# Kernel tuning notes

Measured on AMD Instinct MI355X. Metric: run time of the kernel, lower is better.

## Reference

```python
import jax, jax.numpy as jnp
import numpy as np

EPS = 1e-12  # matches torch F.normalize default eps


def setup_inputs() -> dict:
    key = jax.random.key(0)
    k_x, k_w1, k_b1, k_w2, k_b2 = jax.random.split(key, 5)
    b, n, r, d = 8, 64, 256, 512
    return {
        "x": jax.random.normal(k_x, (b, n, r, d), dtype=jnp.float32),
        "W1": jax.random.normal(k_w1, (d, d), dtype=jnp.float32) * (1.0 / np.sqrt(d)),
        "b1": jax.random.normal(k_b1, (d,), dtype=jnp.float32) * 0.01,
        "W2": jax.random.normal(k_w2, (1, d), dtype=jnp.float32) * (1.0 / np.sqrt(d)),
        "b2": jax.random.normal(k_b2, (1,), dtype=jnp.float32) * 0.01,
    }


def reference(x, W1, b1, W2, b2):
    # F.normalize(x, dim=-1): x / max(||x||_2, eps)
    norm = jnp.sqrt(jnp.sum(x * x, axis=-1, keepdims=True))
    xn = x / jnp.maximum(norm, EPS)                      # [b,n,r,d]
    h = jnp.tanh(jnp.einsum('bnrd,ed->bnre', xn, W1) + b1)  # linear1 + tanh
    scores = (jnp.einsum('bnrd,od->bnro', h, W2) + b2)[..., 0]  # [b,n,r]
    alphas = jax.nn.softmax(scores, axis=2)              # softmax over regions r
    fbar = jnp.einsum('bnr,bnrd->bnd', alphas, xn)       # weighted pooling
    return (fbar, alphas)
```

## Files before the change

### kernel.cpp

```cpp
#include <hip/hip_runtime.h>
#include <hip/hip_bf16.h>

typedef short short8 __attribute__((ext_vector_type(8)));
typedef float floatx4 __attribute__((ext_vector_type(4)));

#define NGROUP 512
#define RREG 256
#define D 512
#define ROWS 131072
#define FBAR_ELEMS (NGROUP * D)

__device__ __forceinline__ unsigned short f2bf(float f) {
    unsigned int u = __float_as_uint(f);
    unsigned int r = (u + 0x7fffu + ((u >> 16) & 1u)) >> 16;
    return (unsigned short)r;
}
__device__ __forceinline__ float fast_tanh(float x) {
    float cx = fminf(fmaxf(x, -9.5f), 9.5f);
    float e  = __builtin_amdgcn_exp2f(cx * 2.8853900817779268f);
    return (e - 1.f) * __builtin_amdgcn_rcpf(e + 1.f);
}

__global__ __launch_bounds__(256) void conv_w1(const float* __restrict__ W1,
                                               unsigned short* __restrict__ W1c) {
    int tid = blockIdx.x * 256 + threadIdx.x;
    int P = tid * 8;
    int kc = P >> 15;
    int L = P & 32767;
    int col = L >> 6;
    int q = L & 63;
    int kl = (q ^ (((col >> 1) & 3) << 4)) >> 1;
    const float* src = W1 + col * 512 + kc * 32 + kl;
    float4 v = *reinterpret_cast<const float4*>(src);
    ushort4 o;
    o.x = f2bf(v.x); o.y = f2bf(v.y); o.z = f2bf(v.z); o.w = f2bf(v.w);
    *reinterpret_cast<ushort4*>((char*)W1c + P) = o;
}

__global__ __launch_bounds__(1024, 8) void score_gemm(
    const float* __restrict__ x, const unsigned short* __restrict__ W1c,
    const float* __restrict__ b1, const float* __restrict__ W2v,
    float* __restrict__ inv_norm, float* __restrict__ scores) {

    __shared__ unsigned short A_lds[2][64 * 32];
    __shared__ unsigned short B_lds[2][512 * 32];
    __shared__ float inv_s[64];

    const int t = threadIdx.x;
    const int lane = t & 63;
    const int w = t >> 6;
    const int cl = lane & 15;
    const int hi = lane >> 4;
    const size_t row0 = (size_t)blockIdx.x * 64;

    auto stageB = [&](int buf, int kc) {
        const char* gb = (const char*)W1c + kc * 32768 + w * 2048 + lane * 16;
        char* lb = (char*)B_lds[buf] + w * 2048;
        #pragma unroll
        for (int i = 0; i < 2; ++i) {
            __builtin_amdgcn_global_load_lds(
                (const __attribute__((address_space(1))) void*)(gb + i * 1024),
                (__attribute__((address_space(3))) void*)(lb + i * 1024),
                16, 0, 0);
        }
    };

    const int arow = t >> 4;
    const int kq = t & 15;
    const int abyte = arow * 64 + ((kq * 4) ^ (((arow >> 1) & 3) << 4));
    const float* xp = x + (row0 + arow) * (size_t)D + kq * 2;

    float ssacc = 0.f;
    auto packA = [&](int buf, float2 v) {
        ssacc += v.x * v.x + v.y * v.y;
        unsigned int pk = (unsigned int)f2bf(v.x) | ((unsigned int)f2bf(v.y) << 16);
        *reinterpret_cast<unsigned int*>((char*)A_lds[buf] + abyte) = pk;
    };

    stageB(0, 0);
    packA(0, *reinterpret_cast<const float2*>(xp));
    __syncthreads();

    floatx4 acc[4][2];
    #pragma unroll
    for (int tt = 0; tt < 4; ++tt) {
        acc[tt][0] = floatx4{0, 0, 0, 0};
        acc[tt][1] = floatx4{0, 0, 0, 0};
    }

    const int fofs = (hi * 16) ^ (((cl >> 1) & 3) << 4);

    #pragma unroll 2
    for (int s = 0; s < 16; ++s) {
        const int cur = s & 1, nx = cur ^ 1;

        float2 xv;
        if (s < 15) {
            xv = *reinterpret_cast<const float2*>(xp + (s + 1) * 32);
            stageB(nx, s + 1);
        }

        short8 bfr0 = *reinterpret_cast<const short8*>(
            (char*)B_lds[cur] + (w * 32 + cl) * 64 + fofs);
        short8 bfr1 = *reinterpret_cast<const short8*>(
            (char*)B_lds[cur] + (w * 32 + 16 + cl) * 64 + fofs);
        #pragma unroll
        for (int tt = 0; tt < 4; ++tt) {
            short8 afr = *reinterpret_cast<const short8*>(
                (char*)A_lds[cur] + (tt * 16 + cl) * 64 + fofs);
            acc[tt][0] = __builtin_amdgcn_mfma_f32_16x16x32_bf16(afr, bfr0, acc[tt][0], 0, 0, 0);
            acc[tt][1] = __builtin_amdgcn_mfma_f32_16x16x32_bf16(afr, bfr1, acc[tt][1], 0, 0, 0);
        }

        if (s < 15) {
            packA(nx, xv);
            __syncthreads();
        }
    }

    ssacc += __shfl_xor(ssacc, 1, 16);
    ssacc += __shfl_xor(ssacc, 2, 16);
    ssacc += __shfl_xor(ssacc, 4, 16);
    ssacc += __shfl_xor(ssacc, 8, 16);
    if (kq == 0) {
        float inv = 1.0f / fmaxf(sqrtf(ssacc), 1e-12f);
        inv_s[arow] = inv;
        inv_norm[row0 + arow] = inv;
    }
    __syncthreads();

    float* scorebuf = (float*)A_lds;

    #pragma unroll
    for (int tt = 0; tt < 4; ++tt) {
        floatx4 iv = *reinterpret_cast<const floatx4*>(&inv_s[tt * 16 + hi * 4]);
        float sp[4] = {0.f, 0.f, 0.f, 0.f};
        #pragma unroll
        for (int f = 0; f < 2; ++f) {
            int col = w * 32 + f * 16 + cl;
            float wv = W2v[col];
            float bb = b1[col];
            #pragma unroll
            for (int i = 0; i < 4; ++i)
                sp[i] += wv * fast_tanh(acc[tt][f][i] * iv[i] + bb);
        }
        #pragma unroll
        for (int i = 0; i < 4; ++i) {
            float v = sp[i];
            v += __shfl_xor(v, 1, 64);
            v += __shfl_xor(v, 2, 64);
            v += __shfl_xor(v, 4, 64);
            v += __shfl_xor(v, 8, 64);
            if (cl == 0) scorebuf[w * 64 + tt * 16 + hi * 4 + i] = v;
        }
    }
    __syncthreads();

    if (t < 64) {
        float s = 0.f;
        #pragma unroll
        for (int q = 0; q < 16; ++q) s += scorebuf[q * 64 + t];
        scores[row0 + t] = s;
    }
}

__global__ __launch_bounds__(512) void softmax_pool(
    const float* __restrict__ x, const float* __restrict__ inv_norm,
    const float* __restrict__ scores, float* __restrict__ out) {

    __shared__ float F[RREG];
    __shared__ float wts[RREG];
    const int t = threadIdx.x;
    const int g = blockIdx.x;

    float s = 0.f, e = 0.f;
    if (t < RREG) { s = scores[g * RREG + t]; F[t] = s; }
    __syncthreads();
    for (int off = 128; off > 0; off >>= 1) {
        if (t < off) F[t] = fmaxf(F[t], F[t + off]);
        __syncthreads();
    }
    float mx = F[0];
    __syncthreads();
    if (t < RREG) { e = expf(s - mx); F[t] = e; }
    __syncthreads();
    for (int off = 128; off > 0; off >>= 1) {
        if (t < off) F[t] += F[t + off];
        __syncthreads();
    }
    float denom = F[0];
    if (t < RREG) {
        float al = e / denom;
        out[FBAR_ELEMS + (size_t)g * RREG + t] = al;
        wts[t] = al * inv_norm[(size_t)g * RREG + t];
    }
    __syncthreads();

    float a = 0.f;
    const float* xb = x + (size_t)g * RREG * D + t;
    #pragma unroll 16
    for (int r = 0; r < RREG; ++r) a += wts[r] * xb[(size_t)r * D];
    out[(size_t)g * D + t] = a;
}

extern "C" void kernel_launch(void* const* d_in, const int* in_sizes, int n_in,
                              void* d_out, int out_size, void* d_ws, size_t ws_size,
                              hipStream_t stream) {
    const float* x  = (const float*)d_in[0];
    const float* W1 = (const float*)d_in[1];
    const float* b1 = (const float*)d_in[2];
    const float* w2 = (const float*)d_in[3];
    float* out = (float*)d_out;

    unsigned short* W1c = (unsigned short*)d_ws;
    float* inv_norm = (float*)((char*)d_ws + 524288);
    float* scores   = (float*)((char*)d_ws + 1048576);

    conv_w1<<<256, 256, 0, stream>>>(W1, W1c);
    score_gemm<<<ROWS / 64, 1024, 0, stream>>>(x, W1c, b1, w2, inv_norm, scores);
    softmax_pool<<<NGROUP, 512, 0, stream>>>(x, inv_norm, scores, out);
}
```

Before: 163.9 us.

## Preload full A tile and triple-buffer W1 without per-step barriers

The score GEMM now loads each block's entire 64x512 x tile up front. It converts the tile to bf16 in LDS and computes the row norms there, instead of streaming A per K-step. W1 chunks are triple-buffered with async global-to-LDS loads, and only s_waitcnt vmcnt is used, which removes the per-iteration __syncthreads. This works because each wave reads only the B region it loaded. The tanh helper is simplified to 1-2/(e+1) without the clamp. The 160KB LDS footprint drops occupancy to one block per CU. All x-load latency is exposed before the MFMA loop, and inv_norm is re-read from global memory right after being written.

```diff
diff --git a/kernel.cpp b/kernel.cpp
--- a/kernel.cpp
+++ b/kernel.cpp
@@ -16,9 +16,8 @@
     return (unsigned short)r;
 }
 __device__ __forceinline__ float fast_tanh(float x) {
-    float cx = fminf(fmaxf(x, -9.5f), 9.5f);
-    float e  = __builtin_amdgcn_exp2f(cx * 2.8853900817779268f);
-    return (e - 1.f) * __builtin_amdgcn_rcpf(e + 1.f);
+    float e = __builtin_amdgcn_exp2f(x * 2.8853900817779268f);
+    return 1.0f - 2.0f * __builtin_amdgcn_rcpf(e + 1.0f);
 }
 
 __global__ __launch_bounds__(256) void conv_w1(const float* __restrict__ W1,
@@ -37,14 +36,13 @@
     *reinterpret_cast<ushort4*>((char*)W1c + P) = o;
 }
 
-__global__ __launch_bounds__(1024, 8) void score_gemm(
+__global__ __launch_bounds__(1024, 4) void score_gemm(
     const float* __restrict__ x, const unsigned short* __restrict__ W1c,
     const float* __restrict__ b1, const float* __restrict__ W2v,
     float* __restrict__ inv_norm, float* __restrict__ scores) {
 
-    __shared__ unsigned short A_lds[2][64 * 32];
-    __shared__ unsigned short B_lds[2][512 * 32];
-    __shared__ float inv_s[64];
+    __shared__ char A_lds[65536];
+    __shared__ char B_lds[3][32768];
 
     const int t = threadIdx.x;
     const int lane = t & 63;
@@ -55,7 +53,7 @@
 
     auto stageB = [&](int buf, int kc) {
         const char* gb = (const char*)W1c + kc * 32768 + w * 2048 + lane * 16;
-        char* lb = (char*)B_lds[buf] + w * 2048;
+        char* lb = &B_lds[buf][w * 2048];
         #pragma unroll
         for (int i = 0; i < 2; ++i) {
             __builtin_amdgcn_global_load_lds(
@@ -65,20 +63,39 @@
         }
     };
 
-    const int arow = t >> 4;
-    const int kq = t & 15;
-    const int abyte = arow * 64 + ((kq * 4) ^ (((arow >> 1) & 3) << 4));
-    const float* xp = x + (row0 + arow) * (size_t)D + kq * 2;
-
-    float ssacc = 0.f;
-    auto packA = [&](int buf, float2 v) {
-        ssacc += v.x * v.x + v.y * v.y;
-        unsigned int pk = (unsigned int)f2bf(v.x) | ((unsigned int)f2bf(v.y) << 16);
-        *reinterpret_cast<unsigned int*>((char*)A_lds[buf] + abyte) = pk;
-    };
-
     stageB(0, 0);
-    packA(0, *reinterpret_cast<const float2*>(xp));
+    stageB(1, 1);
+
+    {
+        const int srow = w * 4 + hi;
+        const int sks = lane & 15;
+        const float* xs = x + (row0 + srow) * (size_t)D + sks * 32;
+        float4 xv[8];
+        #pragma unroll
+        for (int j = 0; j < 8; ++j)
+            xv[j] = *reinterpret_cast<const float4*>(xs + j * 4);
+        float ss = 0.f;
+        #pragma unroll
+        for (int j = 0; j < 8; ++j)
+            ss += xv[j].x*xv[j].x + xv[j].y*xv[j].y + xv[j].z*xv[j].z + xv[j].w*xv[j].w;
+        ss += __shfl_xor(ss, 1, 16);
+        ss += __shfl_xor(ss, 2, 16);
+        ss += __shfl_xor(ss, 4, 16);
+        ss += __shfl_xor(ss, 8, 16);
+        if (sks == 0) inv_norm[row0 + srow] = 1.0f / fmaxf(sqrtf(ss), 1e-12f);
+        const int akey = (srow & 15) << 6;
+        #pragma unroll
+        for (int q = 0; q < 4; ++q) {
+            float4 p = xv[2 * q], r = xv[2 * q + 1];
+            short8 pk;
+            pk[0] = (short)f2bf(p.x); pk[1] = (short)f2bf(p.y);
+            pk[2] = (short)f2bf(p.z); pk[3] = (short)f2bf(p.w);
+            pk[4] = (short)f2bf(r.x); pk[5] = (short)f2bf(r.y);
+            pk[6] = (short)f2bf(r.z); pk[7] = (short)f2bf(r.w);
+            *reinterpret_cast<short8*>(
+                A_lds + srow * 1024 + ((sks * 64 + q * 16) ^ akey)) = pk;
+        }
+    }
     __syncthreads();
 
     floatx4 acc[4][2];
@@ -88,61 +105,44 @@
         acc[tt][1] = floatx4{0, 0, 0, 0};
     }
 
-    const int fofs = (hi * 16) ^ (((cl >> 1) & 3) << 4);
-
-    #pragma unroll 2
+    const int fofsB = (hi * 16) ^ (((cl >> 1) & 3) << 4);
+    const int aoff = cl << 6;
+
+    #pragma unroll
     for (int s = 0; s < 16; ++s) {
-        const int cur = s & 1, nx = cur ^ 1;
-
-        float2 xv;
-        if (s < 15) {
-            xv = *reinterpret_cast<const float2*>(xp + (s + 1) * 32);
-            stageB(nx, s + 1);
-        }
-
-        short8 bfr0 = *reinterpret_cast<const short8*>(
-            (char*)B_lds[cur] + (w * 32 + cl) * 64 + fofs);
-        short8 bfr1 = *reinterpret_cast<const short8*>(
-            (char*)B_lds[cur] + (w * 32 + 16 + cl) * 64 + fofs);
+        if (s + 2 < 16) stageB((s + 2) % 3, s + 2);
+        if (s < 14)       asm volatile("s_waitcnt vmcnt(4)" ::: "memory");
+        else if (s == 14) asm volatile("s_waitcnt vmcnt(2)" ::: "memory");
+        else              asm volatile("s_waitcnt vmcnt(0)" ::: "memory");
+
+        const char* Bb = &B_lds[s % 3][w * 2048];
+        short8 bfr0 = *reinterpret_cast<const short8*>(Bb + cl * 64 + fofsB);
+        short8 bfr1 = *reinterpret_cast<const short8*>(Bb + (16 + cl) * 64 + fofsB);
         #pragma unroll
         for (int tt = 0; tt < 4; ++tt) {
             short8 afr = *reinterpret_cast<const short8*>(
-                (char*)A_lds[cur] + (tt * 16 + cl) * 64 + fofs);
+                A_lds + (tt * 16 + cl) * 1024 + (((s * 64) ^ aoff) + hi * 16));
             acc[tt][0] = __builtin_amdgcn_mfma_f32_16x16x32_bf16(afr, bfr0, acc[tt][0], 0, 0, 0);
             acc[tt][1] = __builtin_amdgcn_mfma_f32_16x16x32_bf16(afr, bfr1, acc[tt][1], 0, 0, 0);
         }
-
-        if (s < 15) {
-            packA(nx, xv);
-            __syncthreads();
-        }
-    }
-
-    ssacc += __shfl_xor(ssacc, 1, 16);
-    ssacc += __shfl_xor(ssacc, 2, 16);
-    ssacc += __shfl_xor(ssacc, 4, 16);
-    ssacc += __shfl_xor(ssacc, 8, 16);
-    if (kq == 0) {
-        float inv = 1.0f / fmaxf(sqrtf(ssacc), 1e-12f);
-        inv_s[arow] = inv;
-        inv_norm[row0 + arow] = inv;
-    }
-    __syncthreads();
-
+    }
+
+    __syncthreads();
     float* scorebuf = (float*)A_lds;
 
     #pragma unroll
     for (int tt = 0; tt < 4; ++tt) {
-        floatx4 iv = *reinterpret_cast<const floatx4*>(&inv_s[tt * 16 + hi * 4]);
+        float4 iv = *reinterpret_cast<const float4*>(inv_norm + row0 + tt * 16 + hi * 4);
         float sp[4] = {0.f, 0.f, 0.f, 0.f};
         #pragma unroll
         for (int f = 0; f < 2; ++f) {
             int col = w * 32 + f * 16 + cl;
             float wv = W2v[col];
             float bb = b1[col];
-            #pragma unroll
-            for (int i = 0; i < 4; ++i)
-                sp[i] += wv * fast_tanh(acc[tt][f][i] * iv[i] + bb);
+            sp[0] += wv * fast_tanh(acc[tt][f][0] * iv.x + bb);
+            sp[1] += wv * fast_tanh(acc[tt][f][1] * iv.y + bb);
+            sp[2] += wv * fast_tanh(acc[tt][f][2] * iv.z + bb);
+            sp[3] += wv * fast_tanh(acc[tt][f][3] * iv.w + bb);
         }
         #pragma unroll
         for (int i = 0; i < 4; ++i) {
@@ -157,10 +157,10 @@
     __syncthreads();
 
     if (t < 64) {
-        float s = 0.f;
-        #pragma unroll
-        for (int q = 0; q < 16; ++q) s += scorebuf[q * 64 + t];
-        scores[row0 + t] = s;
+        float sres = 0.f;
+        #pragma unroll
+        for (int q = 0; q < 16; ++q) sres += scorebuf[q * 64 + t];
+        scores[row0 + t] = sres;
     }
 }
 
```

Measured after the change: 187.0 us. 14.1% more time.
